# Kernel tuning notes

Measured on AMD Instinct MI355X. Metric: run time of the kernel, lower is better.

## Reference

```python
import jax, jax.numpy as jnp
import numpy as np

B, C, H, W = 4, 3, 512, 960
K2 = 16  # 4x4 adaptive filter, DAIN-style


def setup_inputs() -> dict:
    key = jax.random.key(0)
    k1, k2, k3 = jax.random.split(key, 3)
    teninput = jax.random.normal(k1, (B, C, H, W), dtype=jnp.float32)
    tenflow = jax.random.normal(k2, (B, 2, H, W), dtype=jnp.float32)
    tenfilter = jax.random.uniform(k3, (B, K2, H, W), dtype=jnp.float32)
    return {"teninput": teninput, "tenflow": tenflow, "tenfilter": tenfilter}


def reference(teninput, tenflow, tenfilter):
    # DAIN FilterInterpolation forward:
    # out[b,c,y,x] = valid * sum_{dj,di < K} filter[b, dj*K+di, y, x]
    #               * bilinear(input, y2_T + dj + beta, x2_L + di + alpha)
    # with per-corner clamped gathers; out-of-bounds flow targets give 0.
    b, c, h, w = teninput.shape
    k2 = tenfilter.shape[1]
    K = int(np.sqrt(k2))

    dt = teninput.dtype
    xs = jnp.arange(w, dtype=dt)[None, None, :]
    ys = jnp.arange(h, dtype=dt)[None, :, None]
    fx, fy = tenflow[:, 0], tenflow[:, 1]          # [B,H,W]
    x2 = xs + fx
    y2 = ys + fy
    valid = ((x2 >= 0) & (x2 <= w - 1) & (y2 >= 0) & (y2 <= h - 1)
             & (jnp.abs(fx) < w / 2) & (jnp.abs(fy) < h / 2))

    ix = jnp.floor(x2).astype(jnp.int32)
    iy = jnp.floor(y2).astype(jnp.int32)
    alpha = (x2 - ix)[:, None]                     # [B,1,H,W]
    beta = (y2 - iy)[:, None]
    ixL0 = ix + 1 - K // 2                         # window left edge
    iyT0 = iy + 1 - K // 2                         # window top edge

    inp_flat = teninput.reshape(b, c, h * w)

    def gather(yi, xi):  # yi, xi: [B,H,W] int -> [B,C,H,W]
        idx = (yi * w + xi).reshape(b, 1, h * w)
        return jnp.take_along_axis(inp_flat, idx, axis=2).reshape(b, c, h, w)

    wTL = (1 - alpha) * (1 - beta)
    wTR = alpha * (1 - beta)
    wBL = (1 - alpha) * beta
    wBR = alpha * beta

    out = jnp.zeros_like(teninput)
    for dj in range(K):
        yT = jnp.clip(iyT0 + dj, 0, h - 1)
        yB = jnp.clip(iyT0 + dj + 1, 0, h - 1)
        for di in range(K):
            xL = jnp.clip(ixL0 + di, 0, w - 1)
            xR = jnp.clip(ixL0 + di + 1, 0, w - 1)
            val = (wTL * gather(yT, xL) + wTR * gather(yT, xR)
                   + wBL * gather(yB, xL) + wBR * gather(yB, xR))
            out = out + val * tenfilter[:, dj * K + di][:, None]

    return out * valid[:, None].astype(dt)
```

## Files before the change

### kernel.cpp

```cpp
#include <hip/hip_runtime.h>

#define BB 4
#define CC 3
#define HH 512
#define WW 960
#define HW (HH * WW)
#define NPIX (BB * HW)

#define TW 64
#define TH 4
#define NTX (WW / TW)
#define NTY (HH / TH)
#define NBLK (BB * NTX * NTY)

#define ROWS 16
#define COLS 80
#define RSTRIDE (CC * COLS)
#define LDS_FLOATS (ROWS * RSTRIDE)

typedef __attribute__((address_space(1))) const unsigned int gu32;
typedef __attribute__((address_space(3))) unsigned int lu32;

__global__ __launch_bounds__(256)
void filter_interp_kernel(const float* __restrict__ inp,
                          const float* __restrict__ flow,
                          const float* __restrict__ filt,
                          float* __restrict__ out) {
    __shared__ float lds[LDS_FLOATS];

    const int bid = blockIdx.x;
    const int swz = (bid & 7) * (NBLK / 8) + (bid >> 3);
    const int b   = swz / (NTX * NTY);
    const int rr  = swz - b * (NTX * NTY);
    const int tx  = rr / NTY;
    const int ty  = rr - tx * NTY;
    const int x0  = tx * TW;
    const int y0  = ty * TH;

    const int tid  = threadIdx.x;
    const int wave = tid >> 6;
    const float* ibase = inp + (size_t)b * CC * HW;

    if (tx > 0 && tx < NTX - 1) {
#pragma unroll
        for (int e = 0; e < 4; ++e) {
            const int idx = e * 256 + tid;
            if (idx < ROWS * CC * (COLS / 4)) {
                const int s  = idx / 60;
                const int r2 = idx - s * 60;
                const int ch = r2 / 20;
                const int t4 = r2 - ch * 20;
                const int grow = min(max(y0 - 5 + s, 0), HH - 1);
                const float* src = ibase + (size_t)ch * HW +
                                   (size_t)grow * WW + (x0 - 8 + t4 * 4);
                lu32* dst = (lu32*)(void*)&lds[(e * 256 + wave * 64) * 4];
                __builtin_amdgcn_global_load_lds((gu32*)(const void*)src,
                                                 dst, 16, 0, 0);
            }
        }
    } else {
#pragma unroll
        for (int e = 0; e < 15; ++e) {
            const int idx = e * 256 + tid;
            const int s  = idx / RSTRIDE;
            const int r2 = idx - s * RSTRIDE;
            const int ch = r2 / COLS;
            const int t  = r2 - ch * COLS;
            const int grow = min(max(y0 - 5 + s, 0), HH - 1);
            const int gcol = min(max(x0 - 8 + t, 0), WW - 1);
            lds[idx] = ibase[(size_t)ch * HW + (size_t)grow * WW + gcol];
        }
    }

    const int lx = tid & (TW - 1);
    const int wy = tid >> 6;
    const int x  = x0 + lx;
    const int y  = y0 + wy;
    const int rem = y * WW + x;

    const float fx = flow[(size_t)(b * 2 + 0) * HW + rem];
    const float fy = flow[(size_t)(b * 2 + 1) * HW + rem];

    float f[16];
    {
        const float* fptr = filt + (size_t)b * 16 * HW + rem;
#pragma unroll
        for (int k = 0; k < 16; ++k) f[k] = fptr[(size_t)k * HW];
    }

    __syncthreads();

    const float x2 = (float)x + fx;
    const float y2 = (float)y + fy;

    const bool valid = (x2 >= 0.0f) && (x2 <= (float)(WW - 1)) &&
                       (y2 >= 0.0f) && (y2 <= (float)(HH - 1)) &&
                       (fabsf(fx) < (float)WW * 0.5f) &&
                       (fabsf(fy) < (float)HH * 0.5f);

    float acc0 = 0.0f, acc1 = 0.0f, acc2 = 0.0f;

    if (valid) {
        const int ix = (int)floorf(x2);
        const int iy = (int)floorf(y2);
        const float alpha = x2 - (float)ix;
        const float beta  = y2 - (float)iy;

        const float wTL = (1.0f - alpha) * (1.0f - beta);
        const float wTR = alpha * (1.0f - beta);
        const float wBL = (1.0f - alpha) * beta;
        const float wBR = alpha * beta;

        float Wm[5][5];
#pragma unroll
        for (int j = 0; j < 5; ++j)
#pragma unroll
            for (int i = 0; i < 5; ++i) Wm[j][i] = 0.0f;
#pragma unroll
        for (int dj = 0; dj < 4; ++dj) {
#pragma unroll
            for (int di = 0; di < 4; ++di) {
                const float fv = f[dj * 4 + di];
                Wm[dj][di]         += fv * wTL;
                Wm[dj][di + 1]     += fv * wTR;
                Wm[dj + 1][di]     += fv * wBL;
                Wm[dj + 1][di + 1] += fv * wBR;
            }
        }

        const int ixL0 = ix - 1;
        const int iyT0 = iy - 1;
        const int cs = ixL0 - (x0 - 8);
        const int rs = iyT0 - (y0 - 5);

        if ((unsigned)rs <= (unsigned)(ROWS - 5) &&
            (unsigned)cs <= (unsigned)(COLS - 5)) {
            const int o  = cs & 1;
            const int e0 = cs - o;
            const float* lbase = &lds[rs * RSTRIDE + e0];
#pragma unroll
            for (int j = 0; j < 5; ++j) {
                const float* lr = lbase + j * RSTRIDE;
                const float w0 = o ? 0.0f     : Wm[j][0];
                const float w1 = o ? Wm[j][0] : Wm[j][1];
                const float w2 = o ? Wm[j][1] : Wm[j][2];
                const float w3 = o ? Wm[j][2] : Wm[j][3];
                const float w4 = o ? Wm[j][3] : Wm[j][4];
                const float w5 = o ? Wm[j][4] : 0.0f;

                const float2 a0 = *(const float2*)(lr);
                const float2 a1 = *(const float2*)(lr + 2);
                const float2 a2 = *(const float2*)(lr + 4);
                acc0 += a0.x * w0 + a0.y * w1 + a1.x * w2 +
                        a1.y * w3 + a2.x * w4 + a2.y * w5;

                const float2 b0 = *(const float2*)(lr + COLS);
                const float2 b1 = *(const float2*)(lr + COLS + 2);
                const float2 b2 = *(const float2*)(lr + COLS + 4);
                acc1 += b0.x * w0 + b0.y * w1 + b1.x * w2 +
                        b1.y * w3 + b2.x * w4 + b2.y * w5;

                const float2 c0 = *(const float2*)(lr + 2 * COLS);
                const float2 c1 = *(const float2*)(lr + 2 * COLS + 2);
                const float2 c2 = *(const float2*)(lr + 2 * COLS + 4);
                acc2 += c0.x * w0 + c0.y * w1 + c1.x * w2 +
                        c1.y * w3 + c2.x * w4 + c2.y * w5;
            }
        } else {
            int R[5], S[5];
#pragma unroll
            for (int j = 0; j < 5; ++j) R[j] = min(max(iyT0 + j, 0), HH - 1);
#pragma unroll
            for (int i = 0; i < 5; ++i) S[i] = min(max(ixL0 + i, 0), WW - 1);
#pragma unroll
            for (int j = 0; j < 5; ++j) {
                const float* r0 = ibase + (size_t)R[j] * WW;
#pragma unroll
                for (int i = 0; i < 5; ++i) {
                    const float w = Wm[j][i];
                    const size_t oidx = (size_t)S[i];
                    acc0 += r0[oidx] * w;
                    acc1 += r0[HW + oidx] * w;
                    acc2 += r0[2 * (size_t)HW + oidx] * w;
                }
            }
        }
    }

    const int outbase = b * CC * HW + rem;
    out[outbase]          = acc0;
    out[outbase + HW]     = acc1;
    out[outbase + 2 * HW] = acc2;
}

extern "C" void kernel_launch(void* const* d_in, const int* in_sizes, int n_in,
                              void* d_out, int out_size, void* d_ws, size_t ws_size,
                              hipStream_t stream) {
    const float* teninput  = (const float*)d_in[0];
    const float* tenflow   = (const float*)d_in[1];
    const float* tenfilter = (const float*)d_in[2];
    float* out = (float*)d_out;

    filter_interp_kernel<<<NBLK, 256, 0, stream>>>(teninput, tenflow, tenfilter, out);
}
```

Measured before the change: 220.4 us.

## Process two pixel rows per thread with taller tile and padded LDS row stride

Doubles the tile height so each thread computes two output pixels four rows apart, cutting the LDS halo overhead per output from 16 to 20 staged rows for 8 rather than 4 output rows. The LDS row stride is padded to 61 chunks, with filler loads in the interior path, to change bank mapping across rows. Each thread now holds two sets of 16 filter values and two flow pairs, which raises register pressure and halves the block count, at some cost to occupancy and latency hiding.

```diff
diff --git a/kernel.cpp b/kernel.cpp
--- a/kernel.cpp
+++ b/kernel.cpp
@@ -5,21 +5,125 @@
 #define HH 512
 #define WW 960
 #define HW (HH * WW)
-#define NPIX (BB * HW)
 
 #define TW 64
-#define TH 4
+#define TH 8
 #define NTX (WW / TW)
 #define NTY (HH / TH)
 #define NBLK (BB * NTX * NTY)
 
-#define ROWS 16
+#define ROWS 20
 #define COLS 80
-#define RSTRIDE (CC * COLS)
-#define LDS_FLOATS (ROWS * RSTRIDE)
+#define CH_STRIDE 80
+#define CHUNKS_PER_ROW 61
+#define RSTRIDE (CHUNKS_PER_ROW * 4)
+#define DATA_FLOATS_PER_ROW (CC * COLS)
+#define LDS_CHUNKS 1280
+#define LDS_FLOATS (LDS_CHUNKS * 4)
 
 typedef __attribute__((address_space(1))) const unsigned int gu32;
 typedef __attribute__((address_space(3))) unsigned int lu32;
+
+__device__ __forceinline__ void compute_pixel(
+    const float* __restrict__ lds, const float* __restrict__ ibase,
+    int x, int y, int x0, int y0, float fx, float fy,
+    const float* __restrict__ f, float* __restrict__ acc)
+{
+    acc[0] = 0.0f; acc[1] = 0.0f; acc[2] = 0.0f;
+
+    const float x2 = (float)x + fx;
+    const float y2 = (float)y + fy;
+    const bool valid = (x2 >= 0.0f) && (x2 <= (float)(WW - 1)) &&
+                       (y2 >= 0.0f) && (y2 <= (float)(HH - 1)) &&
+                       (fabsf(fx) < (float)WW * 0.5f) &&
+                       (fabsf(fy) < (float)HH * 0.5f);
+    if (!valid) return;
+
+    const int ix = (int)floorf(x2);
+    const int iy = (int)floorf(y2);
+    const float alpha = x2 - (float)ix;
+    const float beta  = y2 - (float)iy;
+
+    const float wTL = (1.0f - alpha) * (1.0f - beta);
+    const float wTR = alpha * (1.0f - beta);
+    const float wBL = (1.0f - alpha) * beta;
+    const float wBR = alpha * beta;
+
+    float Wm[5][5];
+#pragma unroll
+    for (int j = 0; j < 5; ++j)
+#pragma unroll
+        for (int i = 0; i < 5; ++i) Wm[j][i] = 0.0f;
+#pragma unroll
+    for (int dj = 0; dj < 4; ++dj) {
+#pragma unroll
+        for (int di = 0; di < 4; ++di) {
+            const float fv = f[dj * 4 + di];
+            Wm[dj][di]         += fv * wTL;
+            Wm[dj][di + 1]     += fv * wTR;
+            Wm[dj + 1][di]     += fv * wBL;
+            Wm[dj + 1][di + 1] += fv * wBR;
+        }
+    }
+
+    const int ixL0 = ix - 1;
+    const int iyT0 = iy - 1;
+    const int cs = ixL0 - (x0 - 8);
+    const int rs = iyT0 - (y0 - 5);
+
+    if ((unsigned)rs <= (unsigned)(ROWS - 5) &&
+        (unsigned)cs <= (unsigned)(COLS - 5)) {
+        const int o  = cs & 1;
+        const int e0 = cs - o;
+        const float* lbase = lds + rs * RSTRIDE + e0;
+#pragma unroll
+        for (int j = 0; j < 5; ++j) {
+            const float* lr = lbase + j * RSTRIDE;
+            const float w0 = o ? 0.0f     : Wm[j][0];
+            const float w1 = o ? Wm[j][0] : Wm[j][1];
+            const float w2 = o ? Wm[j][1] : Wm[j][2];
+            const float w3 = o ? Wm[j][2] : Wm[j][3];
+            const float w4 = o ? Wm[j][3] : Wm[j][4];
+            const float w5 = o ? Wm[j][4] : 0.0f;
+
+            const float2 a0 = *(const float2*)(lr);
+            const float2 a1 = *(const float2*)(lr + 2);
+            const float2 a2 = *(const float2*)(lr + 4);
+            acc[0] += a0.x * w0 + a0.y * w1 + a1.x * w2 +
+                      a1.y * w3 + a2.x * w4 + a2.y * w5;
+
+            const float2 b0 = *(const float2*)(lr + CH_STRIDE);
+            const float2 b1 = *(const float2*)(lr + CH_STRIDE + 2);
+            const float2 b2 = *(const float2*)(lr + CH_STRIDE + 4);
+            acc[1] += b0.x * w0 + b0.y * w1 + b1.x * w2 +
+                      b1.y * w3 + b2.x * w4 + b2.y * w5;
+
+            const float2 c0 = *(const float2*)(lr + 2 * CH_STRIDE);
+            const float2 c1 = *(const float2*)(lr + 2 * CH_STRIDE + 2);
+            const float2 c2 = *(const float2*)(lr + 2 * CH_STRIDE + 4);
+            acc[2] += c0.x * w0 + c0.y * w1 + c1.x * w2 +
+                      c1.y * w3 + c2.x * w4 + c2.y * w5;
+        }
+    } else {
+        int R[5], S[5];
+#pragma unroll
+        for (int j = 0; j < 5; ++j) R[j] = min(max(iyT0 + j, 0), HH - 1);
+#pragma unroll
+        for (int i = 0; i < 5; ++i) S[i] = min(max(ixL0 + i, 0), WW - 1);
+#pragma unroll
+        for (int j = 0; j < 5; ++j) {
+            const float* r0 = ibase + (size_t)R[j] * WW;
+#pragma unroll
+            for (int i = 0; i < 5; ++i) {
+                const float w = Wm[j][i];
+                const size_t oidx = (size_t)S[i];
+                acc[0] += r0[oidx] * w;
+                acc[1] += r0[HW + oidx] * w;
+                acc[2] += r0[2 * (size_t)HW + oidx] * w;
+            }
+        }
+    }
+}
 
 __global__ __launch_bounds__(256)
 void filter_interp_kernel(const float* __restrict__ inp,
@@ -43,154 +147,74 @@
 
     if (tx > 0 && tx < NTX - 1) {
 #pragma unroll
-        for (int e = 0; e < 4; ++e) {
+        for (int e = 0; e < 5; ++e) {
+            const int u = e * 256 + tid;
+            const int q = u / CHUNKS_PER_ROW;
+            const int r = u - q * CHUNKS_PER_ROW;
+            const int s = min(q, ROWS - 1);
+            int ch, t4;
+            if (r < 60) { ch = r / 20; t4 = r - ch * 20; }
+            else        { ch = 2;      t4 = 19; }
+            const int grow = min(max(y0 - 5 + s, 0), HH - 1);
+            const float* src = ibase + (size_t)ch * HW +
+                               (size_t)grow * WW + (x0 - 8 + t4 * 4);
+            lu32* dst = (lu32*)(void*)&lds[(e * 256 + wave * 64) * 4];
+            __builtin_amdgcn_global_load_lds((gu32*)(const void*)src,
+                                             dst, 16, 0, 0);
+        }
+    } else {
+#pragma unroll
+        for (int e = 0; e < 19; ++e) {
             const int idx = e * 256 + tid;
-            if (idx < ROWS * CC * (COLS / 4)) {
-                const int s  = idx / 60;
-                const int r2 = idx - s * 60;
-                const int ch = r2 / 20;
-                const int t4 = r2 - ch * 20;
+            if (idx < ROWS * DATA_FLOATS_PER_ROW) {
+                const int s   = idx / DATA_FLOATS_PER_ROW;
+                const int rr2 = idx - s * DATA_FLOATS_PER_ROW;
+                const int ch  = rr2 / COLS;
+                const int t   = rr2 - ch * COLS;
                 const int grow = min(max(y0 - 5 + s, 0), HH - 1);
-                const float* src = ibase + (size_t)ch * HW +
-                                   (size_t)grow * WW + (x0 - 8 + t4 * 4);
-                lu32* dst = (lu32*)(void*)&lds[(e * 256 + wave * 64) * 4];
-                __builtin_amdgcn_global_load_lds((gu32*)(const void*)src,
-                                                 dst, 16, 0, 0);
+                const int gcol = min(max(x0 - 8 + t, 0), WW - 1);
+                lds[s * RSTRIDE + rr2] =
+                    ibase[(size_t)ch * HW + (size_t)grow * WW + gcol];
             }
-        }
-    } else {
-#pragma unroll
-        for (int e = 0; e < 15; ++e) {
-            const int idx = e * 256 + tid;
-            const int s  = idx / RSTRIDE;
-            const int r2 = idx - s * RSTRIDE;
-            const int ch = r2 / COLS;
-            const int t  = r2 - ch * COLS;
-            const int grow = min(max(y0 - 5 + s, 0), HH - 1);
-            const int gcol = min(max(x0 - 8 + t, 0), WW - 1);
-            lds[idx] = ibase[(size_t)ch * HW + (size_t)grow * WW + gcol];
         }
     }
 
     const int lx = tid & (TW - 1);
     const int wy = tid >> 6;
-    const int x  = x0 + lx;
-    const int y  = y0 + wy;
-    const int rem = y * WW + x;
-
-    const float fx = flow[(size_t)(b * 2 + 0) * HW + rem];
-    const float fy = flow[(size_t)(b * 2 + 1) * HW + rem];
-
-    float f[16];
+    const int xA = x0 + lx;
+    const int yA = y0 + wy;
+    const int remA = yA * WW + xA;
+    const int remB = remA + 4 * WW;
+
+    const float fxA = flow[(size_t)(b * 2 + 0) * HW + remA];
+    const float fyA = flow[(size_t)(b * 2 + 1) * HW + remA];
+    const float fxB = flow[(size_t)(b * 2 + 0) * HW + remB];
+    const float fyB = flow[(size_t)(b * 2 + 1) * HW + remB];
+
+    float fA[16], fB[16];
     {
-        const float* fptr = filt + (size_t)b * 16 * HW + rem;
-#pragma unroll
-        for (int k = 0; k < 16; ++k) f[k] = fptr[(size_t)k * HW];
+        const float* fpA = filt + (size_t)b * 16 * HW + remA;
+#pragma unroll
+        for (int k = 0; k < 16; ++k) fA[k] = fpA[(size_t)k * HW];
+        const float* fpB = fpA + 4 * WW;
+#pragma unroll
+        for (int k = 0; k < 16; ++k) fB[k] = fpB[(size_t)k * HW];
     }
 
     __syncthreads();
 
-    const float x2 = (float)x + fx;
-    const float y2 = (float)y + fy;
-
-    const bool valid = (x2 >= 0.0f) && (x2 <= (float)(WW - 1)) &&
-                       (y2 >= 0.0f) && (y2 <= (float)(HH - 1)) &&
-                       (fabsf(fx) < (float)WW * 0.5f) &&
-                       (fabsf(fy) < (float)HH * 0.5f);
-
-    float acc0 = 0.0f, acc1 = 0.0f, acc2 = 0.0f;
-
-    if (valid) {
-        const int ix = (int)floorf(x2);
-        const int iy = (int)floorf(y2);
-        const float alpha = x2 - (float)ix;
-        const float beta  = y2 - (float)iy;
-
-        const float wTL = (1.0f - alpha) * (1.0f - beta);
-        const float wTR = alpha * (1.0f - beta);
-        const float wBL = (1.0f - alpha) * beta;
-        const float wBR = alpha * beta;
-
-        float Wm[5][5];
-#pragma unroll
-        for (int j = 0; j < 5; ++j)
-#pragma unroll
-            for (int i = 0; i < 5; ++i) Wm[j][i] = 0.0f;
-#pragma unroll
-        for (int dj = 0; dj < 4; ++dj) {
-#pragma unroll
-            for (int di = 0; di < 4; ++di) {
-                const float fv = f[dj * 4 + di];
-                Wm[dj][di]         += fv * wTL;
-                Wm[dj][di + 1]     += fv * wTR;
-                Wm[dj + 1][di]     += fv * wBL;
-                Wm[dj + 1][di + 1] += fv * wBR;
-            }
-        }
-
-        const int ixL0 = ix - 1;
-        const int iyT0 = iy - 1;
-        const int cs = ixL0 - (x0 - 8);
-        const int rs = iyT0 - (y0 - 5);
-
-        if ((unsigned)rs <= (unsigned)(ROWS - 5) &&
-            (unsigned)cs <= (unsigned)(COLS - 5)) {
-            const int o  = cs & 1;
-            const int e0 = cs - o;
-            const float* lbase = &lds[rs * RSTRIDE + e0];
-#pragma unroll
-            for (int j = 0; j < 5; ++j) {
-                const float* lr = lbase + j * RSTRIDE;
-                const float w0 = o ? 0.0f     : Wm[j][0];
-                const float w1 = o ? Wm[j][0] : Wm[j][1];
-                const float w2 = o ? Wm[j][1] : Wm[j][2];
-                const float w3 = o ? Wm[j][2] : Wm[j][3];
-                const float w4 = o ? Wm[j][3] : Wm[j][4];
-                const float w5 = o ? Wm[j][4] : 0.0f;
-
-                const float2 a0 = *(const float2*)(lr);
-                const float2 a1 = *(const float2*)(lr + 2);
-                const float2 a2 = *(const float2*)(lr + 4);
-                acc0 += a0.x * w0 + a0.y * w1 + a1.x * w2 +
-                        a1.y * w3 + a2.x * w4 + a2.y * w5;
-
-                const float2 b0 = *(const float2*)(lr + COLS);
-                const float2 b1 = *(const float2*)(lr + COLS + 2);
-                const float2 b2 = *(const float2*)(lr + COLS + 4);
-                acc1 += b0.x * w0 + b0.y * w1 + b1.x * w2 +
-                        b1.y * w3 + b2.x * w4 + b2.y * w5;
-
-                const float2 c0 = *(const float2*)(lr + 2 * COLS);
-                const float2 c1 = *(const float2*)(lr + 2 * COLS + 2);
-                const float2 c2 = *(const float2*)(lr + 2 * COLS + 4);
-                acc2 += c0.x * w0 + c0.y * w1 + c1.x * w2 +
-                        c1.y * w3 + c2.x * w4 + c2.y * w5;
-            }
-        } else {
-            int R[5], S[5];
-#pragma unroll
-            for (int j = 0; j < 5; ++j) R[j] = min(max(iyT0 + j, 0), HH - 1);
-#pragma unroll
-            for (int i = 0; i < 5; ++i) S[i] = min(max(ixL0 + i, 0), WW - 1);
-#pragma unroll
-            for (int j = 0; j < 5; ++j) {
-                const float* r0 = ibase + (size_t)R[j] * WW;
-#pragma unroll
-                for (int i = 0; i < 5; ++i) {
-                    const float w = Wm[j][i];
-                    const size_t oidx = (size_t)S[i];
-                    acc0 += r0[oidx] * w;
-                    acc1 += r0[HW + oidx] * w;
-                    acc2 += r0[2 * (size_t)HW + oidx] * w;
-                }
-            }
-        }
-    }
-
-    const int outbase = b * CC * HW + rem;
-    out[outbase]          = acc0;
-    out[outbase + HW]     = acc1;
-    out[outbase + 2 * HW] = acc2;
+    float accA[3], accB[3];
+    compute_pixel(lds, ibase, xA, yA, x0, y0, fxA, fyA, fA, accA);
+    compute_pixel(lds, ibase, xA, yA + 4, x0, y0, fxB, fyB, fB, accB);
+
+    const int obA = b * CC * HW + remA;
+    out[obA]          = accA[0];
+    out[obA + HW]     = accA[1];
+    out[obA + 2 * HW] = accA[2];
+    const int obB = obA + 4 * WW;
+    out[obB]          = accB[0];
+    out[obB + HW]     = accB[1];
+    out[obB + 2 * HW] = accB[2];
 }
 
 extern "C" void kernel_launch(void* const* d_in, const int* in_sizes, int n_in,
```

After: 222.3 us. About the same (+0.9%).

## Process four row tiles per block with staged LDS halo and prefetch pipeline

Applied to the files above, without the earlier changes.

Each block now covers four vertically stacked 64x4 tiles and shares a 28-row LDS halo across them, so overlapping halo rows are loaded once instead of per tile. LDS staging is split into rounds interleaved with double-buffered prefetch of flow and filter values for the next tile, overlapping loads with compute. The trade-off is fewer blocks, more registers for two filter buffers, and a larger LDS footprint, all of which can lower occupancy. A stray no-op read of out[0] is also present.

```diff
diff --git a/kernel.cpp b/kernel.cpp
--- a/kernel.cpp
+++ b/kernel.cpp
@@ -5,18 +5,20 @@
 #define HH 512
 #define WW 960
 #define HW (HH * WW)
-#define NPIX (BB * HW)
 
 #define TW 64
 #define TH 4
 #define NTX (WW / TW)
 #define NTY (HH / TH)
-#define NBLK (BB * NTX * NTY)
-
-#define ROWS 16
-#define COLS 80
-#define RSTRIDE (CC * COLS)
-#define LDS_FLOATS (ROWS * RSTRIDE)
+#define TPB 4
+#define NTYC (NTY / TPB)
+#define NBLK (BB * NTX * NTYC)
+
+#define CHUNKS_PER_ROW 61
+#define RSTRIDE 244
+#define ROWS_TOT 28
+#define LDS_CHUNKS 1792
+#define LDS_FLOATS (LDS_CHUNKS * 4)
 
 typedef __attribute__((address_space(1))) const unsigned int gu32;
 typedef __attribute__((address_space(3))) unsigned int lu32;
@@ -29,168 +31,202 @@
     __shared__ float lds[LDS_FLOATS];
 
     const int bid = blockIdx.x;
-    const int swz = (bid & 7) * (NBLK / 8) + (bid >> 3);
-    const int b   = swz / (NTX * NTY);
-    const int rr  = swz - b * (NTX * NTY);
-    const int tx  = rr / NTY;
-    const int ty  = rr - tx * NTY;
+    const int lid = (bid & 7) * (NBLK / 8) + (bid >> 3);
+    const int b   = lid / (NTX * NTYC);
+    const int rr  = lid - b * (NTX * NTYC);
+    const int tx  = rr / NTYC;
+    const int tyc = rr - tx * NTYC;
     const int x0  = tx * TW;
-    const int y0  = ty * TH;
+    const int y00 = tyc * (TH * TPB);
 
     const int tid  = threadIdx.x;
     const int wave = tid >> 6;
-    const float* ibase = inp + (size_t)b * CC * HW;
-
-    if (tx > 0 && tx < NTX - 1) {
-#pragma unroll
-        for (int e = 0; e < 4; ++e) {
+    const int lx   = tid & 63;
+    const int x    = x0 + lx;
+
+    const float* ibase = inp  + (size_t)b * CC * HW;
+    const float* fbase = filt + (size_t)b * 16 * HW;
+    const float* flbx  = flow + (size_t)(b * 2 + 0) * HW;
+    const float* flby  = flow + (size_t)(b * 2 + 1) * HW;
+    float*       obase = out  + (size_t)b * CC * HW;
+
+    const bool interior = (tx > 0) && (tx < NTX - 1);
+
+    auto stage_round = [&](int u) {
+        const int c   = u * 256 + tid;
+        const int row = c / CHUNKS_PER_ROW;
+        const int cc  = c - row * CHUNKS_PER_ROW;
+        int ch, t4;
+        if (cc < 60) { ch = cc / 20; t4 = cc - ch * 20; }
+        else         { ch = 2;       t4 = 19; }
+        const int grow = min(max(y00 - 5 + row, 0), HH - 1);
+        const float* src = ibase + (size_t)ch * HW +
+                           (size_t)grow * WW + (x0 - 8 + t4 * 4);
+        lu32* dst = (lu32*)(void*)&lds[(u * 256 + wave * 64) * 4];
+        __builtin_amdgcn_global_load_lds((gu32*)(const void*)src, dst, 16, 0, 0);
+    };
+
+    auto stage_scalar = [&](int r0, int nr) {
+        const int total = nr * 240;
+        for (int e = 0; e * 256 < total; ++e) {
             const int idx = e * 256 + tid;
-            if (idx < ROWS * CC * (COLS / 4)) {
-                const int s  = idx / 60;
-                const int r2 = idx - s * 60;
-                const int ch = r2 / 20;
-                const int t4 = r2 - ch * 20;
-                const int grow = min(max(y0 - 5 + s, 0), HH - 1);
-                const float* src = ibase + (size_t)ch * HW +
-                                   (size_t)grow * WW + (x0 - 8 + t4 * 4);
-                lu32* dst = (lu32*)(void*)&lds[(e * 256 + wave * 64) * 4];
-                __builtin_amdgcn_global_load_lds((gu32*)(const void*)src,
-                                                 dst, 16, 0, 0);
+            if (idx < total) {
+                const int r   = idx / 240;
+                const int col = idx - r * 240;
+                const int ch  = col / 80;
+                const int t   = col - ch * 80;
+                const int grow = min(max(y00 - 5 + r0 + r, 0), HH - 1);
+                const int gcol = min(max(x0 - 8 + t, 0), WW - 1);
+                lds[(r0 + r) * RSTRIDE + col] =
+                    ibase[(size_t)ch * HW + (size_t)grow * WW + gcol];
             }
         }
-    } else {
-#pragma unroll
-        for (int e = 0; e < 15; ++e) {
-            const int idx = e * 256 + tid;
-            const int s  = idx / RSTRIDE;
-            const int r2 = idx - s * RSTRIDE;
-            const int ch = r2 / COLS;
-            const int t  = r2 - ch * COLS;
-            const int grow = min(max(y0 - 5 + s, 0), HH - 1);
-            const int gcol = min(max(x0 - 8 + t, 0), WW - 1);
-            lds[idx] = ibase[(size_t)ch * HW + (size_t)grow * WW + gcol];
-        }
-    }
-
-    const int lx = tid & (TW - 1);
-    const int wy = tid >> 6;
-    const int x  = x0 + lx;
-    const int y  = y0 + wy;
-    const int rem = y * WW + x;
-
-    const float fx = flow[(size_t)(b * 2 + 0) * HW + rem];
-    const float fy = flow[(size_t)(b * 2 + 1) * HW + rem];
-
-    float f[16];
-    {
-        const float* fptr = filt + (size_t)b * 16 * HW + rem;
-#pragma unroll
-        for (int k = 0; k < 16; ++k) f[k] = fptr[(size_t)k * HW];
-    }
-
-    __syncthreads();
-
-    const float x2 = (float)x + fx;
-    const float y2 = (float)y + fy;
-
-    const bool valid = (x2 >= 0.0f) && (x2 <= (float)(WW - 1)) &&
-                       (y2 >= 0.0f) && (y2 <= (float)(HH - 1)) &&
-                       (fabsf(fx) < (float)WW * 0.5f) &&
-                       (fabsf(fy) < (float)HH * 0.5f);
-
-    float acc0 = 0.0f, acc1 = 0.0f, acc2 = 0.0f;
-
-    if (valid) {
-        const int ix = (int)floorf(x2);
-        const int iy = (int)floorf(y2);
-        const float alpha = x2 - (float)ix;
-        const float beta  = y2 - (float)iy;
-
-        const float wTL = (1.0f - alpha) * (1.0f - beta);
-        const float wTR = alpha * (1.0f - beta);
-        const float wBL = (1.0f - alpha) * beta;
-        const float wBR = alpha * beta;
-
-        float Wm[5][5];
-#pragma unroll
-        for (int j = 0; j < 5; ++j)
-#pragma unroll
-            for (int i = 0; i < 5; ++i) Wm[j][i] = 0.0f;
-#pragma unroll
-        for (int dj = 0; dj < 4; ++dj) {
-#pragma unroll
-            for (int di = 0; di < 4; ++di) {
-                const float fv = f[dj * 4 + di];
-                Wm[dj][di]         += fv * wTL;
-                Wm[dj][di + 1]     += fv * wTR;
-                Wm[dj + 1][di]     += fv * wBL;
-                Wm[dj + 1][di + 1] += fv * wBR;
+    };
+
+    auto load_pf = [&](int t, float* f, float& pfx, float& pfy, int& prem) {
+        const int y   = y00 + t * TH + wave;
+        const int rem = y * WW + x;
+        prem = rem;
+        pfx = flbx[rem];
+        pfy = flby[rem];
+        const float* fp = fbase + rem;
+#pragma unroll
+        for (int k = 0; k < 16; ++k) f[k] = fp[(size_t)k * HW];
+    };
+
+    auto compute_store = [&](int t, const float* f, float fx, float fy, int rem) {
+        const int y   = y00 + t * TH + wave;
+        const int y0t = y00 + t * TH;
+
+        float acc0 = 0.0f, acc1 = 0.0f, acc2 = 0.0f;
+
+        const float x2 = (float)x + fx;
+        const float y2 = (float)y + fy;
+        const bool valid = (x2 >= 0.0f) && (x2 <= (float)(WW - 1)) &&
+                           (y2 >= 0.0f) && (y2 <= (float)(HH - 1)) &&
+                           (fabsf(fx) < (float)WW * 0.5f) &&
+                           (fabsf(fy) < (float)HH * 0.5f);
+        if (valid) {
+            const int ix = (int)floorf(x2);
+            const int iy = (int)floorf(y2);
+            const float alpha = x2 - (float)ix;
+            const float beta  = y2 - (float)iy;
+
+            const float wTL = (1.0f - alpha) * (1.0f - beta);
+            const float wTR = alpha * (1.0f - beta);
+            const float wBL = (1.0f - alpha) * beta;
+            const float wBR = alpha * beta;
+
+            float Wm[5][5];
+#pragma unroll
+            for (int j = 0; j < 5; ++j)
+#pragma unroll
+                for (int i = 0; i < 5; ++i) Wm[j][i] = 0.0f;
+#pragma unroll
+            for (int dj = 0; dj < 4; ++dj) {
+#pragma unroll
+                for (int di = 0; di < 4; ++di) {
+                    const float fv = f[dj * 4 + di];
+                    Wm[dj][di]         += fv * wTL;
+                    Wm[dj][di + 1]     += fv * wTR;
+                    Wm[dj + 1][di]     += fv * wBL;
+                    Wm[dj + 1][di + 1] += fv * wBR;
+                }
             }
-        }
-
-        const int ixL0 = ix - 1;
-        const int iyT0 = iy - 1;
-        const int cs = ixL0 - (x0 - 8);
-        const int rs = iyT0 - (y0 - 5);
-
-        if ((unsigned)rs <= (unsigned)(ROWS - 5) &&
-            (unsigned)cs <= (unsigned)(COLS - 5)) {
-            const int o  = cs & 1;
-            const int e0 = cs - o;
-            const float* lbase = &lds[rs * RSTRIDE + e0];
-#pragma unroll
-            for (int j = 0; j < 5; ++j) {
-                const float* lr = lbase + j * RSTRIDE;
-                const float w0 = o ? 0.0f     : Wm[j][0];
-                const float w1 = o ? Wm[j][0] : Wm[j][1];
-                const float w2 = o ? Wm[j][1] : Wm[j][2];
-                const float w3 = o ? Wm[j][2] : Wm[j][3];
-                const float w4 = o ? Wm[j][3] : Wm[j][4];
-                const float w5 = o ? Wm[j][4] : 0.0f;
-
-                const float2 a0 = *(const float2*)(lr);
-                const float2 a1 = *(const float2*)(lr + 2);
-                const float2 a2 = *(const float2*)(lr + 4);
-                acc0 += a0.x * w0 + a0.y * w1 + a1.x * w2 +
-                        a1.y * w3 + a2.x * w4 + a2.y * w5;
-
-                const float2 b0 = *(const float2*)(lr + COLS);
-                const float2 b1 = *(const float2*)(lr + COLS + 2);
-                const float2 b2 = *(const float2*)(lr + COLS + 4);
-                acc1 += b0.x * w0 + b0.y * w1 + b1.x * w2 +
-                        b1.y * w3 + b2.x * w4 + b2.y * w5;
-
-                const float2 c0 = *(const float2*)(lr + 2 * COLS);
-                const float2 c1 = *(const float2*)(lr + 2 * COLS + 2);
-                const float2 c2 = *(const float2*)(lr + 2 * COLS + 4);
-                acc2 += c0.x * w0 + c0.y * w1 + c1.x * w2 +
-                        c1.y * w3 + c2.x * w4 + c2.y * w5;
-            }
-        } else {
-            int R[5], S[5];
-#pragma unroll
-            for (int j = 0; j < 5; ++j) R[j] = min(max(iyT0 + j, 0), HH - 1);
-#pragma unroll
-            for (int i = 0; i < 5; ++i) S[i] = min(max(ixL0 + i, 0), WW - 1);
-#pragma unroll
-            for (int j = 0; j < 5; ++j) {
-                const float* r0 = ibase + (size_t)R[j] * WW;
-#pragma unroll
-                for (int i = 0; i < 5; ++i) {
-                    const float w = Wm[j][i];
-                    const size_t oidx = (size_t)S[i];
-                    acc0 += r0[oidx] * w;
-                    acc1 += r0[HW + oidx] * w;
-                    acc2 += r0[2 * (size_t)HW + oidx] * w;
+
+            const int ixL0 = ix - 1;
+            const int iyT0 = iy - 1;
+            const int cs = ixL0 - (x0 - 8);
+            const int rs = iyT0 - (y0t - 5);
+
+            if ((unsigned)rs <= 11u && (unsigned)cs <= 75u) {
+                const int o  = cs & 1;
+                const int e0 = cs - o;
+                const float* lbase = lds + (rs + t * TH) * RSTRIDE + e0;
+#pragma unroll
+                for (int j = 0; j < 5; ++j) {
+                    const float* lr = lbase + j * RSTRIDE;
+                    const float w0 = o ? 0.0f     : Wm[j][0];
+                    const float w1 = o ? Wm[j][0] : Wm[j][1];
+                    const float w2 = o ? Wm[j][1] : Wm[j][2];
+                    const float w3 = o ? Wm[j][2] : Wm[j][3];
+                    const float w4 = o ? Wm[j][3] : Wm[j][4];
+                    const float w5 = o ? Wm[j][4] : 0.0f;
+
+                    const float2 a0 = *(const float2*)(lr);
+                    const float2 a1 = *(const float2*)(lr + 2);
+                    const float2 a2 = *(const float2*)(lr + 4);
+                    acc0 += a0.x * w0 + a0.y * w1 + a1.x * w2 +
+                            a1.y * w3 + a2.x * w4 + a2.y * w5;
+
+                    const float2 b0 = *(const float2*)(lr + 80);
+                    const float2 b1 = *(const float2*)(lr + 82);
+                    const float2 b2 = *(const float2*)(lr + 84);
+                    acc1 += b0.x * w0 + b0.y * w1 + b1.x * w2 +
+                            b1.y * w3 + b2.x * w4 + b2.y * w5;
+
+                    const float2 c0 = *(const float2*)(lr + 160);
+                    const float2 c1 = *(const float2*)(lr + 162);
+                    const float2 c2 = *(const float2*)(lr + 164);
+                    acc2 += c0.x * w0 + c0.y * w1 + c1.x * w2 +
+                            c1.y * w3 + c2.x * w4 + c2.y * w5;
+                }
+            } else {
+                int R[5], S[5];
+#pragma unroll
+                for (int j = 0; j < 5; ++j) R[j] = min(max(iyT0 + j, 0), HH - 1);
+#pragma unroll
+                for (int i = 0; i < 5; ++i) S[i] = min(max(ixL0 + i, 0), WW - 1);
+#pragma unroll
+                for (int j = 0; j < 5; ++j) {
+                    const float* r0p = ibase + (size_t)R[j] * WW;
+#pragma unroll
+                    for (int i = 0; i < 5; ++i) {
+                        const float w = Wm[j][i];
+                        const size_t oo = (size_t)S[i];
+                        acc0 += r0p[oo] * w;
+                        acc1 += r0p[HW + oo] * w;
+                        acc2 += r0p[2 * (size_t)HW + oo] * w;
+                    }
                 }
             }
         }
+
+        out[(size_t)0];
+        obase[rem]            = acc0;
+        obase[rem + HW]       = acc1;
+        obase[rem + 2 * HW]   = acc2;
+    };
+
+    if (interior) {
+        stage_round(0); stage_round(1); stage_round(2);
+        stage_round(3); stage_round(4);
+    } else {
+        stage_scalar(0, 20);
     }
 
-    const int outbase = b * CC * HW + rem;
-    out[outbase]          = acc0;
-    out[outbase + HW]     = acc1;
-    out[outbase + 2 * HW] = acc2;
+    float fA[16], fB[16];
+    float fxA, fyA, fxB, fyB;
+    int remA, remB;
+    load_pf(0, fA, fxA, fyA, remA);
+
+    __syncthreads();
+    if (interior) stage_round(5);
+    else          stage_scalar(20, 4);
+    load_pf(1, fB, fxB, fyB, remB);
+    compute_store(0, fA, fxA, fyA, remA);
+
+    __syncthreads();
+    if (interior) stage_round(6);
+    else          stage_scalar(24, 4);
+    load_pf(2, fA, fxA, fyA, remA);
+    compute_store(1, fB, fxB, fyB, remB);
+
+    __syncthreads();
+    load_pf(3, fB, fxB, fyB, remB);
+    compute_store(2, fA, fxA, fyA, remA);
+
+    compute_store(3, fB, fxB, fyB, remB);
 }
 
 extern "C" void kernel_launch(void* const* d_in, const int* in_sizes, int n_in,
```

After: 224.0 us. About the same (+1.6%).

## Widen tiles to 240x4 with 960-thread blocks and uniform async LDS staging

Applied to the files above, without the earlier changes.

Tiles grow from 64x4 to 240x4 pixels and blocks from 256 to 960 threads. The staged input window becomes 16 rows by 256 columns per channel, with its left edge clamped so every tile, including border tiles, can use the async global-to-LDS 16-byte load path. This drops the scalar fallback load for edge tiles and cuts the halo overfetch per tile. In exchange it needs about 61KB of LDS per block, which limits occupancy, and the large blocks may schedule less flexibly.

```diff
diff --git a/kernel.cpp b/kernel.cpp
--- a/kernel.cpp
+++ b/kernel.cpp
@@ -5,23 +5,26 @@
 #define HH 512
 #define WW 960
 #define HW (HH * WW)
-#define NPIX (BB * HW)
 
-#define TW 64
+#define TW 240
 #define TH 4
 #define NTX (WW / TW)
 #define NTY (HH / TH)
 #define NBLK (BB * NTX * NTY)
+#define NTHREADS 960
 
-#define ROWS 16
-#define COLS 80
-#define RSTRIDE (CC * COLS)
-#define LDS_FLOATS (ROWS * RSTRIDE)
+#define SROWS 16
+#define SCOLS 256
+#define CH_STRIDE 256
+#define CHUNKS_PER_ROW 193
+#define RSTRIDE 772
+#define LDS_CHUNKS (4 * NTHREADS)
+#define LDS_FLOATS (LDS_CHUNKS * 4)
 
 typedef __attribute__((address_space(1))) const unsigned int gu32;
 typedef __attribute__((address_space(3))) unsigned int lu32;
 
-__global__ __launch_bounds__(256)
+__global__ __launch_bounds__(NTHREADS)
 void filter_interp_kernel(const float* __restrict__ inp,
                           const float* __restrict__ flow,
                           const float* __restrict__ filt,
@@ -29,76 +32,66 @@
     __shared__ float lds[LDS_FLOATS];
 
     const int bid = blockIdx.x;
-    const int swz = (bid & 7) * (NBLK / 8) + (bid >> 3);
-    const int b   = swz / (NTX * NTY);
-    const int rr  = swz - b * (NTX * NTY);
-    const int tx  = rr / NTY;
-    const int ty  = rr - tx * NTY;
+    const int lid = (bid & 7) * (NBLK / 8) + (bid >> 3);
+    const int b   = lid >> 9;
+    const int rr  = lid & 511;
+    const int tx  = rr >> 7;
+    const int ty  = rr & 127;
     const int x0  = tx * TW;
     const int y0  = ty * TH;
+    const int sx0 = min(max(x0 - 8, 0), WW - SCOLS);
 
     const int tid  = threadIdx.x;
     const int wave = tid >> 6;
-    const float* ibase = inp + (size_t)b * CC * HW;
 
-    if (tx > 0 && tx < NTX - 1) {
+    const float* ibase = inp  + (size_t)b * CC * HW;
+    const float* fbase = filt + (size_t)b * 16 * HW;
+    const float* flbx  = flow + (size_t)(b * 2 + 0) * HW;
+    const float* flby  = flow + (size_t)(b * 2 + 1) * HW;
+    float*       obase = out  + (size_t)b * CC * HW;
+
 #pragma unroll
-        for (int e = 0; e < 4; ++e) {
-            const int idx = e * 256 + tid;
-            if (idx < ROWS * CC * (COLS / 4)) {
-                const int s  = idx / 60;
-                const int r2 = idx - s * 60;
-                const int ch = r2 / 20;
-                const int t4 = r2 - ch * 20;
-                const int grow = min(max(y0 - 5 + s, 0), HH - 1);
-                const float* src = ibase + (size_t)ch * HW +
-                                   (size_t)grow * WW + (x0 - 8 + t4 * 4);
-                lu32* dst = (lu32*)(void*)&lds[(e * 256 + wave * 64) * 4];
-                __builtin_amdgcn_global_load_lds((gu32*)(const void*)src,
-                                                 dst, 16, 0, 0);
-            }
-        }
-    } else {
-#pragma unroll
-        for (int e = 0; e < 15; ++e) {
-            const int idx = e * 256 + tid;
-            const int s  = idx / RSTRIDE;
-            const int r2 = idx - s * RSTRIDE;
-            const int ch = r2 / COLS;
-            const int t  = r2 - ch * COLS;
-            const int grow = min(max(y0 - 5 + s, 0), HH - 1);
-            const int gcol = min(max(x0 - 8 + t, 0), WW - 1);
-            lds[idx] = ibase[(size_t)ch * HW + (size_t)grow * WW + gcol];
-        }
+    for (int u = 0; u < 4; ++u) {
+        const int c   = u * NTHREADS + tid;
+        const int row = c / CHUNKS_PER_ROW;
+        const int cc  = c - row * CHUNKS_PER_ROW;
+        int ch, t4;
+        if (cc < 192) { ch = cc >> 6; t4 = cc & 63; }
+        else          { ch = 0;       t4 = 0; }
+        const int grow = min(max(y0 - 5 + row, 0), HH - 1);
+        const float* src = ibase + (size_t)ch * HW +
+                           (size_t)grow * WW + (sx0 + t4 * 4);
+        lu32* dst = (lu32*)(void*)&lds[(u * NTHREADS + wave * 64) * 4];
+        __builtin_amdgcn_global_load_lds((gu32*)(const void*)src, dst, 16, 0, 0);
     }
 
-    const int lx = tid & (TW - 1);
-    const int wy = tid >> 6;
-    const int x  = x0 + lx;
-    const int y  = y0 + wy;
+    const int p  = tid;
+    const int py = p / TW;
+    const int px = p - py * TW;
+    const int x  = x0 + px;
+    const int y  = y0 + py;
     const int rem = y * WW + x;
 
-    const float fx = flow[(size_t)(b * 2 + 0) * HW + rem];
-    const float fy = flow[(size_t)(b * 2 + 1) * HW + rem];
+    const float fx = flbx[rem];
+    const float fy = flby[rem];
 
     float f[16];
     {
-        const float* fptr = filt + (size_t)b * 16 * HW + rem;
+        const float* fp = fbase + rem;
 #pragma unroll
-        for (int k = 0; k < 16; ++k) f[k] = fptr[(size_t)k * HW];
+        for (int k = 0; k < 16; ++k) f[k] = fp[(size_t)k * HW];
     }
 
     __syncthreads();
 
+    float acc0 = 0.0f, acc1 = 0.0f, acc2 = 0.0f;
+
     const float x2 = (float)x + fx;
     const float y2 = (float)y + fy;
-
     const bool valid = (x2 >= 0.0f) && (x2 <= (float)(WW - 1)) &&
                        (y2 >= 0.0f) && (y2 <= (float)(HH - 1)) &&
                        (fabsf(fx) < (float)WW * 0.5f) &&
                        (fabsf(fy) < (float)HH * 0.5f);
-
-    float acc0 = 0.0f, acc1 = 0.0f, acc2 = 0.0f;
 
     if (valid) {
         const int ix = (int)floorf(x2);
@@ -130,14 +123,14 @@
 
         const int ixL0 = ix - 1;
         const int iyT0 = iy - 1;
-        const int cs = ixL0 - (x0 - 8);
+        const int cs = ixL0 - sx0;
         const int rs = iyT0 - (y0 - 5);
 
-        if ((unsigned)rs <= (unsigned)(ROWS - 5) &&
-            (unsigned)cs <= (unsigned)(COLS - 5)) {
+        if ((unsigned)rs <= (unsigned)(SROWS - 5) &&
+            (unsigned)cs <= (unsigned)(SCOLS - 6)) {
             const int o  = cs & 1;
             const int e0 = cs - o;
-            const float* lbase = &lds[rs * RSTRIDE + e0];
+            const float* lbase = lds + rs * RSTRIDE + e0;
 #pragma unroll
             for (int j = 0; j < 5; ++j) {
                 const float* lr = lbase + j * RSTRIDE;
@@ -154,15 +147,15 @@
                 acc0 += a0.x * w0 + a0.y * w1 + a1.x * w2 +
                         a1.y * w3 + a2.x * w4 + a2.y * w5;
 
-                const float2 b0 = *(const float2*)(lr + COLS);
-                const float2 b1 = *(const float2*)(lr + COLS + 2);
-                const float2 b2 = *(const float2*)(lr + COLS + 4);
+                const float2 b0 = *(const float2*)(lr + CH_STRIDE);
+                const float2 b1 = *(const float2*)(lr + CH_STRIDE + 2);
+                const float2 b2 = *(const float2*)(lr + CH_STRIDE + 4);
                 acc1 += b0.x * w0 + b0.y * w1 + b1.x * w2 +
                         b1.y * w3 + b2.x * w4 + b2.y * w5;
 
-                const float2 c0 = *(const float2*)(lr + 2 * COLS);
-                const float2 c1 = *(const float2*)(lr + 2 * COLS + 2);
-                const float2 c2 = *(const float2*)(lr + 2 * COLS + 4);
+                const float2 c0 = *(const float2*)(lr + 2 * CH_STRIDE);
+                const float2 c1 = *(const float2*)(lr + 2 * CH_STRIDE + 2);
+                const float2 c2 = *(const float2*)(lr + 2 * CH_STRIDE + 4);
                 acc2 += c0.x * w0 + c0.y * w1 + c1.x * w2 +
                         c1.y * w3 + c2.x * w4 + c2.y * w5;
             }
@@ -174,23 +167,22 @@
             for (int i = 0; i < 5; ++i) S[i] = min(max(ixL0 + i, 0), WW - 1);
 #pragma unroll
             for (int j = 0; j < 5; ++j) {
-                const float* r0 = ibase + (size_t)R[j] * WW;
+                const float* r0p = ibase + (size_t)R[j] * WW;
 #pragma unroll
                 for (int i = 0; i < 5; ++i) {
                     const float w = Wm[j][i];
-                    const size_t oidx = (size_t)S[i];
-                    acc0 += r0[oidx] * w;
-                    acc1 += r0[HW + oidx] * w;
-                    acc2 += r0[2 * (size_t)HW + oidx] * w;
+                    const size_t oo = (size_t)S[i];
+                    acc0 += r0p[oo] * w;
+                    acc1 += r0p[HW + oo] * w;
+                    acc2 += r0p[2 * (size_t)HW + oo] * w;
                 }
             }
         }
     }
 
-    const int outbase = b * CC * HW + rem;
-    out[outbase]          = acc0;
-    out[outbase + HW]     = acc1;
-    out[outbase + 2 * HW] = acc2;
+    obase[rem]          = acc0;
+    obase[rem + HW]     = acc1;
+    obase[rem + 2 * HW] = acc2;
 }
 
 extern "C" void kernel_launch(void* const* d_in, const int* in_sizes, int n_in,
@@ -201,5 +193,5 @@
     const float* tenfilter = (const float*)d_in[2];
     float* out = (float*)d_out;
 
-    filter_interp_kernel<<<NBLK, 256, 0, stream>>>(teninput, tenflow, tenfilter, out);
+    filter_interp_kernel<<<NBLK, NTHREADS, 0, stream>>>(teninput, tenflow, tenfilter, out);
 }
```

Measured after the change: 229.9 us. 1.04x slower.
